# Performance work log

Hardware: AMD Instinct MI355X
Metric: run time of the kernel (lower is better)

## Reference

```python
import jax, jax.numpy as jnp
import numpy as np

B, C, H, W = 256, 3, 224, 224
RETINA = 32
NUM_ZOOM = 3
SCALE = 2
HG, HL = 1024, 256  # num_hidden_glimpse, num_hidden_location
GDIM = NUM_ZOOM * C * RETINA * RETINA  # 9216


def setup_inputs() -> dict:
    key = jax.random.key(0)
    ks = jax.random.split(key, 12)
    images = jax.random.normal(ks[0], (B, C, H, W), dtype=jnp.float32)
    # locations in [-0.4, 0.4] so all multi-scale crops are in-bounds
    locations = (jax.random.uniform(ks[1], (B, 2), dtype=jnp.float32) * 2.0 - 1.0) * 0.4
    def lin(kw, kb, fan_in, fan_out):
        s = 1.0 / np.sqrt(fan_in)
        Wm = jax.random.uniform(kw, (fan_in, fan_out), jnp.float32, -s, s)
        bm = jax.random.uniform(kb, (fan_out,), jnp.float32, -s, s)
        return Wm, bm
    W1, b1 = lin(ks[2], ks[3], GDIM, HG)
    W2, b2 = lin(ks[4], ks[5], 2, HL)
    W3, b3 = lin(ks[6], ks[7], HG, HG + HL)
    W4, b4 = lin(ks[8], ks[9], HL, HG + HL)
    return {"images": images, "locations": locations,
            "W1": W1, "b1": b1, "W2": W2, "b2": b2,
            "W3": W3, "b3": b3, "W4": W4, "b4": b4}


def _foveate(images, locations):
    # images (B,C,H,W); locations (B,2) in [-1,1]
    denorm = (locations + 1.0) * 0.5 * W  # denormalized pixel coords (row, col)
    zoom_patches = []
    for i in range(NUM_ZOOM):
        half = int(RETINA * 0.5 * SCALE ** i)
        size = 2 * half
        def crop(img, loc):
            # int() truncation == floor for in-bounds (non-negative) offsets
            top = jnp.trunc(loc[0] - half).astype(jnp.int32)
            left = jnp.trunc(loc[1] - half).astype(jnp.int32)
            return jax.lax.dynamic_slice(img, (jnp.int32(0), top, left), (C, size, size))
        crops = jax.vmap(crop)(images, denorm)  # (B,C,size,size)
        resized = jax.image.resize(crops, (crops.shape[0], C, RETINA, RETINA),
                                   method="bilinear", antialias=False)
        zoom_patches.append(resized)
    g = jnp.stack(zoom_patches, axis=1)  # (B, Z, C, r, r)
    return g.reshape(g.shape[0], -1)  # (B, Z*C*r*r)


def reference(images, locations, W1, b1, W2, b2, W3, b3, W4, b4):
    g = _foveate(images, locations)
    hg = jax.nn.relu(jax.nn.relu(g @ W1 + b1) @ W3 + b3)
    hl = jax.nn.relu(jax.nn.relu(locations @ W2 + b2) @ W4 + b4)
    return jax.nn.relu(hg + hl)
```

## Files before the change

kernel.cpp:

```cpp
#include <hip/hip_runtime.h>

typedef __attribute__((ext_vector_type(8))) short short8;
typedef __attribute__((ext_vector_type(16))) float f32x16;

#define Bsz 256
#define Cch 3
#define Him 224
#define Wim 224
#define RET 32
#define HG 1024
#define HL 256
#define GDIM 9216
#define NOUT 1280

__device__ __forceinline__ unsigned short f2bf(float x) {
  unsigned u = __float_as_uint(x);
  return (unsigned short)((u + 0x7fffu + ((u >> 16) & 1u)) >> 16);
}
__device__ __forceinline__ float bf2f(unsigned short h) {
  return __uint_as_float((unsigned)h << 16);
}

__global__ __launch_bounds__(256) void foveate_kernel(
    const float* __restrict__ img, const float* __restrict__ loc,
    unsigned short* __restrict__ ghi, unsigned short* __restrict__ glo) {
  int idx = blockIdx.x * 256 + threadIdx.x;
  int b = idx / GDIM;
  int r = idx - b * GDIM;
  int z = r / (Cch * RET * RET);
  int r2 = r - z * (Cch * RET * RET);
  int c = r2 / (RET * RET);
  int p = r2 - c * (RET * RET);
  int i = p >> 5, j = p & 31;
  float dr = (loc[b * 2 + 0] + 1.f) * .5f * (float)Wim;
  float dc = (loc[b * 2 + 1] + 1.f) * .5f * (float)Wim;
  int half = 16 << z;
  int top = (int)truncf(dr - (float)half), left = (int)truncf(dc - (float)half);
  const float* base = img + ((long)b * Cch + c) * (Him * Wim);
  float v;
  if (z == 0) {
    v = base[(top + i) * Wim + left + j];
  } else {
    int rr = (z == 1) ? top + 2 * i : top + 4 * i + 1;
    int cc = (z == 1) ? left + 2 * j : left + 4 * j + 1;
    v = .25f * (base[rr * Wim + cc] + base[rr * Wim + cc + 1] +
                base[(rr + 1) * Wim + cc] + base[(rr + 1) * Wim + cc + 1]);
  }
  unsigned short h = f2bf(v);
  int off = (r >> 3) * 2048 + b * 8 + (r & 7);
  ghi[off] = h;
  glo[off] = f2bf(v - bf2f(h));
}

__global__ __launch_bounds__(256) void tconv_kernel(
    const float* __restrict__ in, unsigned short* __restrict__ oh,
    unsigned short* __restrict__ ol, int K, int N) {
  __shared__ float tile[32][33];
  int n0 = blockIdx.x * 32, k0 = blockIdx.y * 32;
  int r = threadIdx.x >> 3, c4 = (threadIdx.x & 7) * 4;
  float4 v = *(const float4*)(in + (long)(k0 + r) * N + n0 + c4);
  tile[r][c4 + 0] = v.x; tile[r][c4 + 1] = v.y;
  tile[r][c4 + 2] = v.z; tile[r][c4 + 3] = v.w;
  __syncthreads();
  if (threadIdx.x < 128) {
    int rr = threadIdx.x >> 2, c8 = (threadIdx.x & 3) * 8;
    unsigned hi01 = 0, hi23 = 0, hi45 = 0, hi67 = 0;
    unsigned lo01 = 0, lo23 = 0, lo45 = 0, lo67 = 0;
    unsigned hh[8], ll[8];
#pragma unroll
    for (int j = 0; j < 8; ++j) {
      float x = tile[c8 + j][rr];
      hh[j] = f2bf(x);
      ll[j] = f2bf(x - bf2f((unsigned short)hh[j]));
    }
    hi01 = hh[0] | (hh[1] << 16); hi23 = hh[2] | (hh[3] << 16);
    hi45 = hh[4] | (hh[5] << 16); hi67 = hh[6] | (hh[7] << 16);
    lo01 = ll[0] | (ll[1] << 16); lo23 = ll[2] | (ll[3] << 16);
    lo45 = ll[4] | (ll[5] << 16); lo67 = ll[6] | (ll[7] << 16);
    long off = (long)((k0 + c8) >> 3) * (N * 8) + (n0 + rr) * 8;
    *(uint4*)(oh + off) = make_uint4(hi01, hi23, hi45, hi67);
    *(uint4*)(ol + off) = make_uint4(lo01, lo23, lo45, lo67);
  }
}

__device__ __forceinline__ void gemm_core(
    const unsigned short* __restrict__ Ahi, const unsigned short* __restrict__ Alo,
    const unsigned short* __restrict__ Bhi, const unsigned short* __restrict__ Blo,
    int Bn, int n0, int kblk0, int iters, f32x16 acc[2][4],
    unsigned short* __restrict__ lds) {
  const int t = threadIdx.x, w = t >> 6, lane = t & 63;
  const int l5 = lane & 31, lh = lane >> 5;
  unsigned short* lAh = lds;
  unsigned short* lAl = lds + 8192;
  unsigned short* lBh = lds + 16384;
  unsigned short* lBl = lds + 20480;

  uint4 rAh[4], rAl[4], rBh[2], rBl[2];
  long aoff[4], boff[2];
#pragma unroll
  for (int q = 0; q < 4; ++q) aoff[q] = (long)kblk0 * 2048 + (q * 256 + t) * 8;
#pragma unroll
  for (int q = 0; q < 2; ++q) {
    int s = q * 256 + t;
    boff[q] = ((long)kblk0 + (s >> 7)) * Bn * 8 + (long)(n0 + (s & 127)) * 8;
  }
#pragma unroll
  for (int q = 0; q < 4; ++q) {
    rAh[q] = *(const uint4*)(Ahi + aoff[q]);
    rAl[q] = *(const uint4*)(Alo + aoff[q]);
  }
#pragma unroll
  for (int q = 0; q < 2; ++q) {
    rBh[q] = *(const uint4*)(Bhi + boff[q]);
    rBl[q] = *(const uint4*)(Blo + boff[q]);
  }

  for (int it = 0; it < iters; ++it) {
    __syncthreads();
#pragma unroll
    for (int q = 0; q < 4; ++q) {
      *(uint4*)(lAh + (q * 256 + t) * 8) = rAh[q];
      *(uint4*)(lAl + (q * 256 + t) * 8) = rAl[q];
    }
#pragma unroll
    for (int q = 0; q < 2; ++q) {
      *(uint4*)(lBh + (q * 256 + t) * 8) = rBh[q];
      *(uint4*)(lBl + (q * 256 + t) * 8) = rBl[q];
    }
    __syncthreads();
    if (it + 1 < iters) {
      long ka = (long)(it + 1) * 8192;
      long kb = (long)(it + 1) * 4 * Bn * 8;
#pragma unroll
      for (int q = 0; q < 4; ++q) {
        rAh[q] = *(const uint4*)(Ahi + aoff[q] + ka);
        rAl[q] = *(const uint4*)(Alo + aoff[q] + ka);
      }
#pragma unroll
      for (int q = 0; q < 2; ++q) {
        rBh[q] = *(const uint4*)(Bhi + boff[q] + kb);
        rBl[q] = *(const uint4*)(Blo + boff[q] + kb);
      }
    }
#pragma unroll
    for (int ks = 0; ks < 2; ++ks) {
      short8 fa[2][2], fb[2][4];
#pragma unroll
      for (int mi = 0; mi < 2; ++mi) {
        int off = ((ks * 2 + lh) * 256 + w * 64 + mi * 32 + l5) * 8;
        fa[0][mi] = *(const short8*)(lAh + off);
        fa[1][mi] = *(const short8*)(lAl + off);
      }
#pragma unroll
      for (int ni = 0; ni < 4; ++ni) {
        int off = ((ks * 2 + lh) * 128 + ni * 32 + l5) * 8;
        fb[0][ni] = *(const short8*)(lBh + off);
        fb[1][ni] = *(const short8*)(lBl + off);
      }
#pragma unroll
      for (int mi = 0; mi < 2; ++mi)
#pragma unroll
        for (int ni = 0; ni < 4; ++ni)
          acc[mi][ni] = __builtin_amdgcn_mfma_f32_32x32x16_bf16(fa[0][mi], fb[0][ni], acc[mi][ni], 0, 0, 0);
#pragma unroll
      for (int mi = 0; mi < 2; ++mi)
#pragma unroll
        for (int ni = 0; ni < 4; ++ni)
          acc[mi][ni] = __builtin_amdgcn_mfma_f32_32x32x16_bf16(fa[0][mi], fb[1][ni], acc[mi][ni], 0, 0, 0);
#pragma unroll
      for (int mi = 0; mi < 2; ++mi)
#pragma unroll
        for (int ni = 0; ni < 4; ++ni)
          acc[mi][ni] = __builtin_amdgcn_mfma_f32_32x32x16_bf16(fa[1][mi], fb[0][ni], acc[mi][ni], 0, 0, 0);
    }
  }
}

__device__ __forceinline__ void epilogue(float* __restrict__ Pz, int ldp, int n0,
                                         f32x16 acc[2][4]) {
  const int t = threadIdx.x, w = t >> 6, lane = t & 63;
  const int l5 = lane & 31, lh = lane >> 5;
#pragma unroll
  for (int mi = 0; mi < 2; ++mi)
#pragma unroll
    for (int ni = 0; ni < 4; ++ni) {
      int col = n0 + ni * 32 + l5;
      int rbase = w * 64 + mi * 32 + 4 * lh;
#pragma unroll
      for (int r = 0; r < 16; ++r) {
        int row = rbase + (r & 3) + 8 * (r >> 2);
        Pz[(long)row * ldp + col] = acc[mi][ni][r];
      }
    }
}

__global__ __launch_bounds__(256, 1) void gemm1_kernel(
    const unsigned short* __restrict__ ghi, const unsigned short* __restrict__ glo,
    const unsigned short* __restrict__ w1hi, const unsigned short* __restrict__ w1lo,
    float* __restrict__ P) {
  __shared__ __align__(16) unsigned short lds[24576];
  f32x16 acc[2][4];
#pragma unroll
  for (int i = 0; i < 2; ++i)
#pragma unroll
    for (int j = 0; j < 4; ++j)
#pragma unroll
      for (int r = 0; r < 16; ++r) acc[i][j][r] = 0.f;
  int n0 = blockIdx.x * 128, z = blockIdx.y;
  gemm_core(ghi, glo, w1hi, w1lo, HG, n0, z * 36, 9, acc, lds);
  epilogue(P + (long)z * Bsz * HG, HG, n0, acc);
}

__global__ __launch_bounds__(256, 1) void gemm2_kernel(
    const unsigned short* __restrict__ h1hi, const unsigned short* __restrict__ h1lo,
    const unsigned short* __restrict__ h2hi, const unsigned short* __restrict__ h2lo,
    const unsigned short* __restrict__ w3hi, const unsigned short* __restrict__ w3lo,
    const unsigned short* __restrict__ w4hi, const unsigned short* __restrict__ w4lo,
    float* __restrict__ P) {
  __shared__ __align__(16) unsigned short lds[24576];
  f32x16 acc[2][4];
#pragma unroll
  for (int i = 0; i < 2; ++i)
#pragma unroll
    for (int j = 0; j < 4; ++j)
#pragma unroll
      for (int r = 0; r < 16; ++r) acc[i][j][r] = 0.f;
  int n0 = blockIdx.x * 128, z = blockIdx.y;
  if (z < 8)
    gemm_core(h1hi, h1lo, w3hi, w3lo, NOUT, n0, z * 16, 4, acc, lds);
  else
    gemm_core(h2hi, h2lo, w4hi, w4lo, NOUT, n0, (z - 8) * 16, 4, acc, lds);
  epilogue(P + (long)z * Bsz * NOUT, NOUT, n0, acc);
}

__global__ __launch_bounds__(256) void reduce1_h2_kernel(
    const float* __restrict__ P, const float* __restrict__ b1,
    const float* __restrict__ loc, const float* __restrict__ W2,
    const float* __restrict__ b2,
    unsigned short* __restrict__ h1hi, unsigned short* __restrict__ h1lo,
    unsigned short* __restrict__ h2hi, unsigned short* __restrict__ h2lo) {
  if (blockIdx.x < 256) {
    int i4 = (blockIdx.x * 256 + threadIdx.x) * 4;
    float4 s = *(const float4*)(P + i4);
    for (int z = 1; z < 32; ++z) {
      float4 p = *(const float4*)(P + (long)z * (Bsz * HG) + i4);
      s.x += p.x; s.y += p.y; s.z += p.z; s.w += p.w;
    }
    int m = i4 >> 10, k = i4 & (HG - 1);
    float4 bb = *(const float4*)(b1 + k);
    float v0 = fmaxf(s.x + bb.x, 0.f), v1 = fmaxf(s.y + bb.y, 0.f);
    float v2 = fmaxf(s.z + bb.z, 0.f), v3 = fmaxf(s.w + bb.w, 0.f);
    unsigned short h0 = f2bf(v0), h1 = f2bf(v1), h2 = f2bf(v2), h3 = f2bf(v3);
    int off = (k >> 3) * 2048 + m * 8 + (k & 7);
    *(ushort4*)(h1hi + off) = make_ushort4(h0, h1, h2, h3);
    *(ushort4*)(h1lo + off) = make_ushort4(f2bf(v0 - bf2f(h0)), f2bf(v1 - bf2f(h1)),
                                           f2bf(v2 - bf2f(h2)), f2bf(v3 - bf2f(h3)));
  } else {
    int i4 = ((blockIdx.x - 256) * 256 + threadIdx.x) * 4;
    int b = i4 >> 8, k = i4 & (HL - 1);
    float l0 = loc[b * 2 + 0], l1 = loc[b * 2 + 1];
    float4 w0 = *(const float4*)(W2 + k);
    float4 w1 = *(const float4*)(W2 + HL + k);
    float4 bb = *(const float4*)(b2 + k);
    float v0 = fmaxf(fmaf(l0, w0.x, fmaf(l1, w1.x, bb.x)), 0.f);
    float v1 = fmaxf(fmaf(l0, w0.y, fmaf(l1, w1.y, bb.y)), 0.f);
    float v2 = fmaxf(fmaf(l0, w0.z, fmaf(l1, w1.z, bb.z)), 0.f);
    float v3 = fmaxf(fmaf(l0, w0.w, fmaf(l1, w1.w, bb.w)), 0.f);
    unsigned short h0 = f2bf(v0), h1 = f2bf(v1), h2 = f2bf(v2), h3 = f2bf(v3);
    int off = (k >> 3) * 2048 + b * 8 + (k & 7);
    *(ushort4*)(h2hi + off) = make_ushort4(h0, h1, h2, h3);
    *(ushort4*)(h2lo + off) = make_ushort4(f2bf(v0 - bf2f(h0)), f2bf(v1 - bf2f(h1)),
                                           f2bf(v2 - bf2f(h2)), f2bf(v3 - bf2f(h3)));
  }
}

__global__ __launch_bounds__(256) void reduce2_kernel(
    const float* __restrict__ P, const float* __restrict__ b3,
    const float* __restrict__ b4, float* __restrict__ out) {
  int i4 = (blockIdx.x * 256 + threadIdx.x) * 4;
  float4 a = *(const float4*)(P + i4);
  for (int z = 1; z < 8; ++z) {
    float4 p = *(const float4*)(P + (long)z * (Bsz * NOUT) + i4);
    a.x += p.x; a.y += p.y; a.z += p.z; a.w += p.w;
  }
  float4 c8 = *(const float4*)(P + 8L * (Bsz * NOUT) + i4);
  float4 c9 = *(const float4*)(P + 9L * (Bsz * NOUT) + i4);
  int n = i4 % NOUT;
  float4 b3v = *(const float4*)(b3 + n);
  float4 b4v = *(const float4*)(b4 + n);
  float4 o;
  o.x = fmaxf(fmaxf(a.x + b3v.x, 0.f) + fmaxf(c8.x + c9.x + b4v.x, 0.f), 0.f);
  o.y = fmaxf(fmaxf(a.y + b3v.y, 0.f) + fmaxf(c8.y + c9.y + b4v.y, 0.f), 0.f);
  o.z = fmaxf(fmaxf(a.z + b3v.z, 0.f) + fmaxf(c8.z + c9.z + b4v.z, 0.f), 0.f);
  o.w = fmaxf(fmaxf(a.w + b3v.w, 0.f) + fmaxf(c8.w + c9.w + b4v.w, 0.f), 0.f);
  *(float4*)(out + i4) = o;
}

extern "C" void kernel_launch(void* const* d_in, const int* in_sizes, int n_in,
                              void* d_out, int out_size, void* d_ws, size_t ws_size,
                              hipStream_t stream) {
  const float* images = (const float*)d_in[0];
  const float* locs = (const float*)d_in[1];
  const float* W1 = (const float*)d_in[2];
  const float* b1 = (const float*)d_in[3];
  const float* W2 = (const float*)d_in[4];
  const float* b2 = (const float*)d_in[5];
  const float* W3 = (const float*)d_in[6];
  const float* b3 = (const float*)d_in[7];
  const float* W4 = (const float*)d_in[8];
  const float* b4 = (const float*)d_in[9];
  float* out = (float*)d_out;

  unsigned short* p = (unsigned short*)d_ws;
  unsigned short* gsh = p; p += 2359296;
  unsigned short* gsl = p; p += 2359296;
  unsigned short* w1h = p; p += 9437184;
  unsigned short* w1l = p; p += 9437184;
  unsigned short* w3h = p; p += 1310720;
  unsigned short* w3l = p; p += 1310720;
  unsigned short* w4h = p; p += 327680;
  unsigned short* w4l = p; p += 327680;
  unsigned short* h1h = p; p += 262144;
  unsigned short* h1l = p; p += 262144;
  unsigned short* h2h = p; p += 65536;
  unsigned short* h2l = p; p += 65536;
  float* P1 = (float*)p;
  float* P2 = P1 + 8388608;

  tconv_kernel<<<dim3(HG / 32, GDIM / 32), 256, 0, stream>>>(W1, w1h, w1l, GDIM, HG);
  tconv_kernel<<<dim3(NOUT / 32, HG / 32), 256, 0, stream>>>(W3, w3h, w3l, HG, NOUT);
  tconv_kernel<<<dim3(NOUT / 32, HL / 32), 256, 0, stream>>>(W4, w4h, w4l, HL, NOUT);
  foveate_kernel<<<(Bsz * GDIM) / 256, 256, 0, stream>>>(images, locs, gsh, gsl);
  gemm1_kernel<<<dim3(8, 32), 256, 0, stream>>>(gsh, gsl, w1h, w1l, P1);
  reduce1_h2_kernel<<<320, 256, 0, stream>>>(P1, b1, locs, W2, b2, h1h, h1l, h2h, h2l);
  gemm2_kernel<<<dim3(10, 10), 256, 0, stream>>>(h1h, h1l, h2h, h2l, w3h, w3l, w4h, w4l, P2);
  reduce2_kernel<<<(Bsz * NOUT) / 1024, 256, 0, stream>>>(P2, b3, b4, out);
}
```

Before: 330.4 us.

## Retile GEMMs to 128x128 blocks with 2x2 warp layout and more split-K

The GEMM core tile changes from 256x128 to 128x128 with a 2x2 wave arrangement, adds an M-block grid dimension, and raises launch bounds to two blocks per CU. Gemm2 doubles its split-K factor, and the final reduction sums 20 partial slabs instead of 10. The three weight-conversion launches merge into one kernel. The aim is more blocks in flight, better occupancy and fewer launches. The cost is extra global traffic from reloading A/B tiles per M-block and a larger partial-sum buffer.

```diff
diff --git a/kernel.cpp b/kernel.cpp
--- a/kernel.cpp
+++ b/kernel.cpp
@@ -52,11 +52,20 @@
   glo[off] = f2bf(v - bf2f(h));
 }
 
-__global__ __launch_bounds__(256) void tconv_kernel(
-    const float* __restrict__ in, unsigned short* __restrict__ oh,
-    unsigned short* __restrict__ ol, int K, int N) {
+__global__ __launch_bounds__(256) void tconv_all_kernel(
+    const float* __restrict__ W1, unsigned short* __restrict__ w1h, unsigned short* __restrict__ w1l,
+    const float* __restrict__ W3, unsigned short* __restrict__ w3h, unsigned short* __restrict__ w3l,
+    const float* __restrict__ W4, unsigned short* __restrict__ w4h, unsigned short* __restrict__ w4l) {
   __shared__ float tile[32][33];
-  int n0 = blockIdx.x * 32, k0 = blockIdx.y * 32;
+  int bx = blockIdx.x;
+  const float* in;
+  unsigned short *oh, *ol;
+  int K, N, lb;
+  if (bx < 9216)       { in = W1; oh = w1h; ol = w1l; K = GDIM; N = HG;   lb = bx; }
+  else if (bx < 10496) { in = W3; oh = w3h; ol = w3l; K = HG;   N = NOUT; lb = bx - 9216; }
+  else                 { in = W4; oh = w4h; ol = w4l; K = HL;   N = NOUT; lb = bx - 10496; }
+  int nb = N >> 5;
+  int n0 = (lb % nb) * 32, k0 = (lb / nb) * 32;
   int r = threadIdx.x >> 3, c4 = (threadIdx.x & 7) * 4;
   float4 v = *(const float4*)(in + (long)(k0 + r) * N + n0 + c4);
   tile[r][c4 + 0] = v.x; tile[r][c4 + 1] = v.y;
@@ -64,8 +73,6 @@
   __syncthreads();
   if (threadIdx.x < 128) {
     int rr = threadIdx.x >> 2, c8 = (threadIdx.x & 3) * 8;
-    unsigned hi01 = 0, hi23 = 0, hi45 = 0, hi67 = 0;
-    unsigned lo01 = 0, lo23 = 0, lo45 = 0, lo67 = 0;
     unsigned hh[8], ll[8];
 #pragma unroll
     for (int j = 0; j < 8; ++j) {
@@ -73,44 +80,42 @@
       hh[j] = f2bf(x);
       ll[j] = f2bf(x - bf2f((unsigned short)hh[j]));
     }
-    hi01 = hh[0] | (hh[1] << 16); hi23 = hh[2] | (hh[3] << 16);
-    hi45 = hh[4] | (hh[5] << 16); hi67 = hh[6] | (hh[7] << 16);
-    lo01 = ll[0] | (ll[1] << 16); lo23 = ll[2] | (ll[3] << 16);
-    lo45 = ll[4] | (ll[5] << 16); lo67 = ll[6] | (ll[7] << 16);
     long off = (long)((k0 + c8) >> 3) * (N * 8) + (n0 + rr) * 8;
-    *(uint4*)(oh + off) = make_uint4(hi01, hi23, hi45, hi67);
-    *(uint4*)(ol + off) = make_uint4(lo01, lo23, lo45, lo67);
+    *(uint4*)(oh + off) = make_uint4(hh[0] | (hh[1] << 16), hh[2] | (hh[3] << 16),
+                                     hh[4] | (hh[5] << 16), hh[6] | (hh[7] << 16));
+    *(uint4*)(ol + off) = make_uint4(ll[0] | (ll[1] << 16), ll[2] | (ll[3] << 16),
+                                     ll[4] | (ll[5] << 16), ll[6] | (ll[7] << 16));
   }
 }
 
 __device__ __forceinline__ void gemm_core(
     const unsigned short* __restrict__ Ahi, const unsigned short* __restrict__ Alo,
+    int Mtot, int m0,
     const unsigned short* __restrict__ Bhi, const unsigned short* __restrict__ Blo,
-    int Bn, int n0, int kblk0, int iters, f32x16 acc[2][4],
-    unsigned short* __restrict__ lds) {
-  const int t = threadIdx.x, w = t >> 6, lane = t & 63;
+    int Ntot, int n0,
+    int kblk0, int iters, f32x16 acc[2][2], unsigned short* __restrict__ lds) {
+  const int t = threadIdx.x, lane = t & 63;
+  const int wm = t >> 7, wn = (t >> 6) & 1;
   const int l5 = lane & 31, lh = lane >> 5;
   unsigned short* lAh = lds;
-  unsigned short* lAl = lds + 8192;
-  unsigned short* lBh = lds + 16384;
-  unsigned short* lBl = lds + 20480;
-
-  uint4 rAh[4], rAl[4], rBh[2], rBl[2];
-  long aoff[4], boff[2];
-#pragma unroll
-  for (int q = 0; q < 4; ++q) aoff[q] = (long)kblk0 * 2048 + (q * 256 + t) * 8;
+  unsigned short* lAl = lds + 4096;
+  unsigned short* lBh = lds + 8192;
+  unsigned short* lBl = lds + 12288;
+
+  long aoff[2], boff[2];
 #pragma unroll
   for (int q = 0; q < 2; ++q) {
     int s = q * 256 + t;
-    boff[q] = ((long)kblk0 + (s >> 7)) * Bn * 8 + (long)(n0 + (s & 127)) * 8;
-  }
-#pragma unroll
-  for (int q = 0; q < 4; ++q) {
+    int kb = s >> 7, rr = s & 127;
+    aoff[q] = ((long)(kblk0 + kb) * Mtot + m0 + rr) * 8;
+    boff[q] = ((long)(kblk0 + kb) * Ntot + n0 + rr) * 8;
+  }
+  const long da4 = (long)4 * Mtot * 8, db4 = (long)4 * Ntot * 8;
+  uint4 rAh[2], rAl[2], rBh[2], rBl[2];
+#pragma unroll
+  for (int q = 0; q < 2; ++q) {
     rAh[q] = *(const uint4*)(Ahi + aoff[q]);
     rAl[q] = *(const uint4*)(Alo + aoff[q]);
-  }
-#pragma unroll
-  for (int q = 0; q < 2; ++q) {
     rBh[q] = *(const uint4*)(Bhi + boff[q]);
     rBl[q] = *(const uint4*)(Blo + boff[q]);
   }
@@ -118,74 +123,69 @@
   for (int it = 0; it < iters; ++it) {
     __syncthreads();
 #pragma unroll
-    for (int q = 0; q < 4; ++q) {
-      *(uint4*)(lAh + (q * 256 + t) * 8) = rAh[q];
-      *(uint4*)(lAl + (q * 256 + t) * 8) = rAl[q];
-    }
-#pragma unroll
     for (int q = 0; q < 2; ++q) {
-      *(uint4*)(lBh + (q * 256 + t) * 8) = rBh[q];
-      *(uint4*)(lBl + (q * 256 + t) * 8) = rBl[q];
+      int d = (q * 256 + t) * 8;
+      *(uint4*)(lAh + d) = rAh[q];
+      *(uint4*)(lAl + d) = rAl[q];
+      *(uint4*)(lBh + d) = rBh[q];
+      *(uint4*)(lBl + d) = rBl[q];
     }
     __syncthreads();
     if (it + 1 < iters) {
-      long ka = (long)(it + 1) * 8192;
-      long kb = (long)(it + 1) * 4 * Bn * 8;
-#pragma unroll
-      for (int q = 0; q < 4; ++q) {
-        rAh[q] = *(const uint4*)(Ahi + aoff[q] + ka);
-        rAl[q] = *(const uint4*)(Alo + aoff[q] + ka);
+#pragma unroll
+      for (int q = 0; q < 2; ++q) {
+        aoff[q] += da4; boff[q] += db4;
+        rAh[q] = *(const uint4*)(Ahi + aoff[q]);
+        rAl[q] = *(const uint4*)(Alo + aoff[q]);
+        rBh[q] = *(const uint4*)(Bhi + boff[q]);
+        rBl[q] = *(const uint4*)(Blo + boff[q]);
       }
-#pragma unroll
-      for (int q = 0; q < 2; ++q) {
-        rBh[q] = *(const uint4*)(Bhi + boff[q] + kb);
-        rBl[q] = *(const uint4*)(Blo + boff[q] + kb);
+    }
+#pragma unroll
+    for (int ks = 0; ks < 2; ++ks) {
+      short8 fah[2], fal[2], fbh[2], fbl[2];
+#pragma unroll
+      for (int mi = 0; mi < 2; ++mi) {
+        int off = ((ks * 2 + lh) * 128 + wm * 64 + mi * 32 + l5) * 8;
+        fah[mi] = *(const short8*)(lAh + off);
+        fal[mi] = *(const short8*)(lAl + off);
       }
-    }
-#pragma unroll
-    for (int ks = 0; ks < 2; ++ks) {
-      short8 fa[2][2], fb[2][4];
-#pragma unroll
-      for (int mi = 0; mi < 2; ++mi) {
-        int off = ((ks * 2 + lh) * 256 + w * 64 + mi * 32 + l5) * 8;
-        fa[0][mi] = *(const short8*)(lAh + off);
-        fa[1][mi] = *(const short8*)(lAl + off);
+#pragma unroll
+      for (int ni = 0; ni < 2; ++ni) {
+        int off = ((ks * 2 + lh) * 128 + wn * 64 + ni * 32 + l5) * 8;
+        fbh[ni] = *(const short8*)(lBh + off);
+        fbl[ni] = *(const short8*)(lBl + off);
       }
 #pragma unroll
-      for (int ni = 0; ni < 4; ++ni) {
-        int off = ((ks * 2 + lh) * 128 + ni * 32 + l5) * 8;
-        fb[0][ni] = *(const short8*)(lBh + off);
-        fb[1][ni] = *(const short8*)(lBl + off);
-      }
-#pragma unroll
       for (int mi = 0; mi < 2; ++mi)
 #pragma unroll
-        for (int ni = 0; ni < 4; ++ni)
-          acc[mi][ni] = __builtin_amdgcn_mfma_f32_32x32x16_bf16(fa[0][mi], fb[0][ni], acc[mi][ni], 0, 0, 0);
+        for (int ni = 0; ni < 2; ++ni)
+          acc[mi][ni] = __builtin_amdgcn_mfma_f32_32x32x16_bf16(fah[mi], fbh[ni], acc[mi][ni], 0, 0, 0);
 #pragma unroll
       for (int mi = 0; mi < 2; ++mi)
 #pragma unroll
-        for (int ni = 0; ni < 4; ++ni)
-          acc[mi][ni] = __builtin_amdgcn_mfma_f32_32x32x16_bf16(fa[0][mi], fb[1][ni], acc[mi][ni], 0, 0, 0);
+        for (int ni = 0; ni < 2; ++ni)
+          acc[mi][ni] = __builtin_amdgcn_mfma_f32_32x32x16_bf16(fah[mi], fbl[ni], acc[mi][ni], 0, 0, 0);
 #pragma unroll
       for (int mi = 0; mi < 2; ++mi)
 #pragma unroll
-        for (int ni = 0; ni < 4; ++ni)
-          acc[mi][ni] = __builtin_amdgcn_mfma_f32_32x32x16_bf16(fa[1][mi], fb[0][ni], acc[mi][ni], 0, 0, 0);
-    }
-  }
-}
-
-__device__ __forceinline__ void epilogue(float* __restrict__ Pz, int ldp, int n0,
-                                         f32x16 acc[2][4]) {
-  const int t = threadIdx.x, w = t >> 6, lane = t & 63;
+        for (int ni = 0; ni < 2; ++ni)
+          acc[mi][ni] = __builtin_amdgcn_mfma_f32_32x32x16_bf16(fal[mi], fbh[ni], acc[mi][ni], 0, 0, 0);
+    }
+  }
+}
+
+__device__ __forceinline__ void epilogue(float* __restrict__ Pz, int ldp, int m0,
+                                         int n0, f32x16 acc[2][2]) {
+  const int t = threadIdx.x, lane = t & 63;
+  const int wm = t >> 7, wn = (t >> 6) & 1;
   const int l5 = lane & 31, lh = lane >> 5;
 #pragma unroll
   for (int mi = 0; mi < 2; ++mi)
 #pragma unroll
-    for (int ni = 0; ni < 4; ++ni) {
-      int col = n0 + ni * 32 + l5;
-      int rbase = w * 64 + mi * 32 + 4 * lh;
+    for (int ni = 0; ni < 2; ++ni) {
+      int col = n0 + wn * 64 + ni * 32 + l5;
+      int rbase = m0 + wm * 64 + mi * 32 + 4 * lh;
 #pragma unroll
       for (int r = 0; r < 16; ++r) {
         int row = rbase + (r & 3) + 8 * (r >> 2);
@@ -194,51 +194,51 @@
     }
 }
 
-__global__ __launch_bounds__(256, 1) void gemm1_kernel(
+__global__ __launch_bounds__(256, 2) void gemm1_kernel(
     const unsigned short* __restrict__ ghi, const unsigned short* __restrict__ glo,
-    const unsigned short* __restrict__ w1hi, const unsigned short* __restrict__ w1lo,
+    const unsigned short* __restrict__ w1h, const unsigned short* __restrict__ w1l,
     float* __restrict__ P) {
-  __shared__ __align__(16) unsigned short lds[24576];
-  f32x16 acc[2][4];
+  __shared__ __align__(16) unsigned short lds[16384];
+  f32x16 acc[2][2];
 #pragma unroll
   for (int i = 0; i < 2; ++i)
 #pragma unroll
-    for (int j = 0; j < 4; ++j)
+    for (int j = 0; j < 2; ++j)
 #pragma unroll
       for (int r = 0; r < 16; ++r) acc[i][j][r] = 0.f;
-  int n0 = blockIdx.x * 128, z = blockIdx.y;
-  gemm_core(ghi, glo, w1hi, w1lo, HG, n0, z * 36, 9, acc, lds);
-  epilogue(P + (long)z * Bsz * HG, HG, n0, acc);
-}
-
-__global__ __launch_bounds__(256, 1) void gemm2_kernel(
-    const unsigned short* __restrict__ h1hi, const unsigned short* __restrict__ h1lo,
-    const unsigned short* __restrict__ h2hi, const unsigned short* __restrict__ h2lo,
-    const unsigned short* __restrict__ w3hi, const unsigned short* __restrict__ w3lo,
-    const unsigned short* __restrict__ w4hi, const unsigned short* __restrict__ w4lo,
+  int n0 = blockIdx.x * 128, m0 = blockIdx.y * 128, z = blockIdx.z;
+  gemm_core(ghi, glo, Bsz, m0, w1h, w1l, HG, n0, z * 36, 9, acc, lds);
+  epilogue(P + (long)z * Bsz * HG, HG, m0, n0, acc);
+}
+
+__global__ __launch_bounds__(256, 2) void gemm2_kernel(
+    const unsigned short* __restrict__ h1h, const unsigned short* __restrict__ h1l,
+    const unsigned short* __restrict__ h2h, const unsigned short* __restrict__ h2l,
+    const unsigned short* __restrict__ w3h, const unsigned short* __restrict__ w3l,
+    const unsigned short* __restrict__ w4h, const unsigned short* __restrict__ w4l,
     float* __restrict__ P) {
-  __shared__ __align__(16) unsigned short lds[24576];
-  f32x16 acc[2][4];
+  __shared__ __align__(16) unsigned short lds[16384];
+  f32x16 acc[2][2];
 #pragma unroll
   for (int i = 0; i < 2; ++i)
 #pragma unroll
-    for (int j = 0; j < 4; ++j)
+    for (int j = 0; j < 2; ++j)
 #pragma unroll
       for (int r = 0; r < 16; ++r) acc[i][j][r] = 0.f;
-  int n0 = blockIdx.x * 128, z = blockIdx.y;
-  if (z < 8)
-    gemm_core(h1hi, h1lo, w3hi, w3lo, NOUT, n0, z * 16, 4, acc, lds);
+  int n0 = blockIdx.x * 128, m0 = blockIdx.y * 128, z = blockIdx.z;
+  if (z < 16)
+    gemm_core(h1h, h1l, Bsz, m0, w3h, w3l, NOUT, n0, z * 8, 2, acc, lds);
   else
-    gemm_core(h2hi, h2lo, w4hi, w4lo, NOUT, n0, (z - 8) * 16, 4, acc, lds);
-  epilogue(P + (long)z * Bsz * NOUT, NOUT, n0, acc);
+    gemm_core(h2h, h2l, Bsz, m0, w4h, w4l, NOUT, n0, (z - 16) * 8, 2, acc, lds);
+  epilogue(P + (long)z * Bsz * NOUT, NOUT, m0, n0, acc);
 }
 
 __global__ __launch_bounds__(256) void reduce1_h2_kernel(
     const float* __restrict__ P, const float* __restrict__ b1,
     const float* __restrict__ loc, const float* __restrict__ W2,
     const float* __restrict__ b2,
-    unsigned short* __restrict__ h1hi, unsigned short* __restrict__ h1lo,
-    unsigned short* __restrict__ h2hi, unsigned short* __restrict__ h2lo) {
+    unsigned short* __restrict__ h1h, unsigned short* __restrict__ h1l,
+    unsigned short* __restrict__ h2h, unsigned short* __restrict__ h2l) {
   if (blockIdx.x < 256) {
     int i4 = (blockIdx.x * 256 + threadIdx.x) * 4;
     float4 s = *(const float4*)(P + i4);
@@ -252,9 +252,9 @@
     float v2 = fmaxf(s.z + bb.z, 0.f), v3 = fmaxf(s.w + bb.w, 0.f);
     unsigned short h0 = f2bf(v0), h1 = f2bf(v1), h2 = f2bf(v2), h3 = f2bf(v3);
     int off = (k >> 3) * 2048 + m * 8 + (k & 7);
-    *(ushort4*)(h1hi + off) = make_ushort4(h0, h1, h2, h3);
-    *(ushort4*)(h1lo + off) = make_ushort4(f2bf(v0 - bf2f(h0)), f2bf(v1 - bf2f(h1)),
-                                           f2bf(v2 - bf2f(h2)), f2bf(v3 - bf2f(h3)));
+    *(ushort4*)(h1h + off) = make_ushort4(h0, h1, h2, h3);
+    *(ushort4*)(h1l + off) = make_ushort4(f2bf(v0 - bf2f(h0)), f2bf(v1 - bf2f(h1)),
+                                          f2bf(v2 - bf2f(h2)), f2bf(v3 - bf2f(h3)));
   } else {
     int i4 = ((blockIdx.x - 256) * 256 + threadIdx.x) * 4;
     int b = i4 >> 8, k = i4 & (HL - 1);
@@ -268,9 +268,9 @@
     float v3 = fmaxf(fmaf(l0, w0.w, fmaf(l1, w1.w, bb.w)), 0.f);
     unsigned short h0 = f2bf(v0), h1 = f2bf(v1), h2 = f2bf(v2), h3 = f2bf(v3);
     int off = (k >> 3) * 2048 + b * 8 + (k & 7);
-    *(ushort4*)(h2hi + off) = make_ushort4(h0, h1, h2, h3);
-    *(ushort4*)(h2lo + off) = make_ushort4(f2bf(v0 - bf2f(h0)), f2bf(v1 - bf2f(h1)),
-                                           f2bf(v2 - bf2f(h2)), f2bf(v3 - bf2f(h3)));
+    *(ushort4*)(h2h + off) = make_ushort4(h0, h1, h2, h3);
+    *(ushort4*)(h2l + off) = make_ushort4(f2bf(v0 - bf2f(h0)), f2bf(v1 - bf2f(h1)),
+                                          f2bf(v2 - bf2f(h2)), f2bf(v3 - bf2f(h3)));
   }
 }
 
@@ -278,21 +278,25 @@
     const float* __restrict__ P, const float* __restrict__ b3,
     const float* __restrict__ b4, float* __restrict__ out) {
   int i4 = (blockIdx.x * 256 + threadIdx.x) * 4;
+  const long S = (long)Bsz * NOUT;
   float4 a = *(const float4*)(P + i4);
-  for (int z = 1; z < 8; ++z) {
-    float4 p = *(const float4*)(P + (long)z * (Bsz * NOUT) + i4);
+  for (int z = 1; z < 16; ++z) {
+    float4 p = *(const float4*)(P + z * S + i4);
     a.x += p.x; a.y += p.y; a.z += p.z; a.w += p.w;
   }
-  float4 c8 = *(const float4*)(P + 8L * (Bsz * NOUT) + i4);
-  float4 c9 = *(const float4*)(P + 9L * (Bsz * NOUT) + i4);
+  float4 c = *(const float4*)(P + 16 * S + i4);
+  for (int z = 17; z < 20; ++z) {
+    float4 p = *(const float4*)(P + z * S + i4);
+    c.x += p.x; c.y += p.y; c.z += p.z; c.w += p.w;
+  }
   int n = i4 % NOUT;
   float4 b3v = *(const float4*)(b3 + n);
   float4 b4v = *(const float4*)(b4 + n);
   float4 o;
-  o.x = fmaxf(fmaxf(a.x + b3v.x, 0.f) + fmaxf(c8.x + c9.x + b4v.x, 0.f), 0.f);
-  o.y = fmaxf(fmaxf(a.y + b3v.y, 0.f) + fmaxf(c8.y + c9.y + b4v.y, 0.f), 0.f);
-  o.z = fmaxf(fmaxf(a.z + b3v.z, 0.f) + fmaxf(c8.z + c9.z + b4v.z, 0.f), 0.f);
-  o.w = fmaxf(fmaxf(a.w + b3v.w, 0.f) + fmaxf(c8.w + c9.w + b4v.w, 0.f), 0.f);
+  o.x = fmaxf(fmaxf(a.x + b3v.x, 0.f) + fmaxf(c.x + b4v.x, 0.f), 0.f);
+  o.y = fmaxf(fmaxf(a.y + b3v.y, 0.f) + fmaxf(c.y + b4v.y, 0.f), 0.f);
+  o.z = fmaxf(fmaxf(a.z + b3v.z, 0.f) + fmaxf(c.z + b4v.z, 0.f), 0.f);
+  o.w = fmaxf(fmaxf(a.w + b3v.w, 0.f) + fmaxf(c.w + b4v.w, 0.f), 0.f);
   *(float4*)(out + i4) = o;
 }
 
@@ -327,12 +331,10 @@
   float* P1 = (float*)p;
   float* P2 = P1 + 8388608;
 
-  tconv_kernel<<<dim3(HG / 32, GDIM / 32), 256, 0, stream>>>(W1, w1h, w1l, GDIM, HG);
-  tconv_kernel<<<dim3(NOUT / 32, HG / 32), 256, 0, stream>>>(W3, w3h, w3l, HG, NOUT);
-  tconv_kernel<<<dim3(NOUT / 32, HL / 32), 256, 0, stream>>>(W4, w4h, w4l, HL, NOUT);
+  tconv_all_kernel<<<10816, 256, 0, stream>>>(W1, w1h, w1l, W3, w3h, w3l, W4, w4h, w4l);
   foveate_kernel<<<(Bsz * GDIM) / 256, 256, 0, stream>>>(images, locs, gsh, gsl);
-  gemm1_kernel<<<dim3(8, 32), 256, 0, stream>>>(gsh, gsl, w1h, w1l, P1);
+  gemm1_kernel<<<dim3(8, 2, 32), 256, 0, stream>>>(gsh, gsl, w1h, w1l, P1);
   reduce1_h2_kernel<<<320, 256, 0, stream>>>(P1, b1, locs, W2, b2, h1h, h1l, h2h, h2l);
-  gemm2_kernel<<<dim3(10, 10), 256, 0, stream>>>(h1h, h1l, h2h, h2l, w3h, w3l, w4h, w4l, P2);
+  gemm2_kernel<<<dim3(10, 2, 20), 256, 0, stream>>>(h1h, h1l, h2h, h2l, w3h, w3l, w4h, w4l, P2);
   reduce2_kernel<<<(Bsz * NOUT) / 1024, 256, 0, stream>>>(P2, b3, b4, out);
 }
```

After: 329.2 us. Within noise of the previous version (-0.4%).
